# Kernel optimization log

Measured on AMD Instinct MI355X. Metric: run time of the kernel, lower is better.

## Reference

```python
import jax, jax.numpy as jnp
import numpy as np

N, C, S = 16, 512, 4096

def setup_inputs() -> dict:
    rng = jax.random.key(0)
    k1, k2, k3 = jax.random.split(rng, 3)
    return {
        "key": jax.random.normal(k1, (N, C, S), dtype=jnp.float32),
        "value": jax.random.normal(k2, (N, C, S), dtype=jnp.float32),
        "query": jax.random.normal(k3, (N, C, S), dtype=jnp.float32),
    }

def reference(key, value, query):
    KC = key.shape[1]
    # query.permute(0,2,1): [N, C, S] -> [N, S, C]
    # sim_map = bmm(key, query^T): [N, C, C], scaled by KC^-0.5
    sim = jnp.einsum("ncs,nds->ncd", key, query) * (KC ** -0.5)
    # softmax over dim=1 (first C axis)
    sim = jax.nn.softmax(sim, axis=1)
    # context = bmm(sim, value): [N, C, C] @ [N, C, S] -> [N, C, S]
    context = jnp.einsum("ncd,nds->ncs", sim, value)
    return context
```

## Files before the change

kernel.cpp:

```cpp
#include <hip/hip_runtime.h>

typedef __bf16 bf16x8 __attribute__((ext_vector_type(8)));
typedef float f32x4 __attribute__((ext_vector_type(4)));
typedef unsigned short u16;
typedef u16 u16x4 __attribute__((ext_vector_type(4)));
typedef u16 u16x8 __attribute__((ext_vector_type(8)));

__device__ __forceinline__ u16 f2bf(float f) {
  unsigned u = __builtin_bit_cast(unsigned, f);
  unsigned r = (u + 0x7fffu + ((u >> 16) & 1u)) >> 16;
  return (u16)r;
}

__device__ __forceinline__ void gld_lds16(const u16* g, u16* l) {
  __builtin_amdgcn_global_load_lds(
      (__attribute__((address_space(1))) void*)(g),
      (__attribute__((address_space(3))) void*)(l), 16, 0, 0);
}

__device__ __forceinline__ f32x4 ntload4(const float* p) {
  return __builtin_nontemporal_load((const f32x4*)p);
}

__global__ __launch_bounds__(256) void k_cvt(const float* __restrict__ K,
                                             const float* __restrict__ Q,
                                             u16* __restrict__ Kb,
                                             u16* __restrict__ Qb) {
  const float* src = blockIdx.y ? Q : K;
  u16* dst = blockIdx.y ? Qb : Kb;
  const size_t base = (size_t)blockIdx.x * 4096;
  const int t = threadIdx.x;
  f32x4 v[4];
#pragma unroll
  for (int c = 0; c < 4; ++c)
    v[c] = ntload4(src + base + c * 1024 + t * 4);
#pragma unroll
  for (int c = 0; c < 4; ++c) {
    u16x4 h;
    h[0] = f2bf(v[c][0]); h[1] = f2bf(v[c][1]); h[2] = f2bf(v[c][2]); h[3] = f2bf(v[c][3]);
    *(u16x4*)(dst + base + c * 1024 + t * 4) = h;
  }
}

__global__ __launch_bounds__(512) void k_mix(const u16* __restrict__ Kb,
                                             const u16* __restrict__ Qb,
                                             float* __restrict__ Lp,
                                             const float* __restrict__ V,
                                             u16* __restrict__ Vt) {
  extern __shared__ char raw[];
  const int bid = blockIdx.x;
  const int t = threadIdx.x;

  if (bid % 5 == 0) {
    u16* sA = (u16*)raw;
    u16* sB = (u16*)(raw + 32768);
    const int sid0 = bid / 5;
    const int sid = (sid0 & 7) * 64 + (sid0 >> 3);
    const int n = sid >> 5;
    const int rem = sid & 31;
    const int kc = rem >> 4;
    const int r2 = rem & 15;
    const int cy = r2 >> 2, dx = r2 & 3;
    const int lane = t & 63, wid = t >> 6;
    const int wr = wid >> 2, wc = wid & 3;
    const float scale = 0.04419417382415922f;

    const u16* Ab = Kb + ((size_t)n * 512 + cy * 128) * 4096 + kc * 2048;
    const u16* Bb = Qb + ((size_t)n * 512 + dx * 128) * 4096 + kc * 2048;
    f32x4 acc[4][2] = {};
    const int srow0 = t >> 3;
    const int scol = ((t & 7) << 3) ^ ((srow0 & 7) << 3);

#define MIX_STAGE(buf, k0)                                                      \
  {                                                                             \
    _Pragma("unroll") for (int q = 0; q < 2; ++q) {                             \
      const int row = q * 64 + srow0;                                           \
      gld_lds16(Ab + (size_t)row * 4096 + (k0) + scol,                          \
                sA + (buf) * 8192 + (q * 512 + (wid << 6)) * 8);                \
      gld_lds16(Bb + (size_t)row * 4096 + (k0) + scol,                          \
                sB + (buf) * 8192 + (q * 512 + (wid << 6)) * 8);                \
    }                                                                           \
  }
#define MIX_COMPUTE(buf)                                                        \
  {                                                                             \
    _Pragma("unroll") for (int ki = 0; ki < 2; ++ki) {                          \
      bf16x8 a[4], b[2];                                                        \
      const int ce = ki * 32 + (lane >> 4) * 8;                                 \
      _Pragma("unroll") for (int mi = 0; mi < 4; ++mi) {                        \
        const int r = wr * 64 + mi * 16 + (lane & 15);                          \
        a[mi] = *(const bf16x8*)&sA[(buf) * 8192 + r * 64 + (ce ^ ((r & 7) << 3))]; \
      }                                                                         \
      _Pragma("unroll") for (int ni = 0; ni < 2; ++ni) {                        \
        const int r = wc * 32 + ni * 16 + (lane & 15);                          \
        b[ni] = *(const bf16x8*)&sB[(buf) * 8192 + r * 64 + (ce ^ ((r & 7) << 3))]; \
      }                                                                         \
      __builtin_amdgcn_s_setprio(1);                                            \
      _Pragma("unroll") for (int mi = 0; mi < 4; ++mi)                          \
        _Pragma("unroll") for (int ni = 0; ni < 2; ++ni)                        \
          acc[mi][ni] = __builtin_amdgcn_mfma_f32_16x16x32_bf16(                \
              a[mi], b[ni], acc[mi][ni], 0, 0, 0);                              \
      __builtin_amdgcn_s_setprio(0);                                            \
    }                                                                           \
  }

    MIX_STAGE(0, 0);
    __syncthreads();
    int cur = 0;
    for (int kt = 0; kt < 31; ++kt) {
      MIX_STAGE(cur ^ 1, (kt + 1) << 6);
      MIX_COMPUTE(cur);
      __syncthreads();
      cur ^= 1;
    }
    MIX_COMPUTE(cur);

    float* Lb = Lp + ((size_t)kc * 16 + n) * 512 * 512;
    const int c0 = cy * 128, d0 = dx * 128;
#pragma unroll
    for (int mi = 0; mi < 4; ++mi)
#pragma unroll
      for (int ni = 0; ni < 2; ++ni) {
        int colo = d0 + wc * 32 + ni * 16 + (lane & 15);
#pragma unroll
        for (int j = 0; j < 4; ++j) {
          int rowo = c0 + wr * 64 + mi * 16 + ((lane >> 4) << 2) + j;
          Lb[(size_t)rowo * 512 + colo] = acc[mi][ni][j] * scale;
        }
      }
#undef MIX_STAGE
#undef MIX_COMPUTE
  } else {
    const int vid = bid - bid / 5 - 1;
    const int sub = t >> 8, tt = t & 255;
    const int tile = vid * 2 + sub;
    const int n = tile >> 8;
    const int r = tile & 255;
    const int d0 = (r >> 6) * 128, s0 = (r & 63) * 64;
    float* lds = (float*)(raw + sub * 34816);
    {
      const int r0 = tt >> 4, c4 = (tt & 15) << 2;
#pragma unroll
      for (int p = 0; p < 8; ++p) {
        const int dr = r0 + p * 16;
        f32x4 v = ntload4(V + ((size_t)n * 512 + d0 + dr) * 4096 + s0 + c4);
        const int sw = ((dr >> 3) & 7) << 2;
        *(f32x4*)(&lds[dr * 68 + (c4 ^ sw)]) = v;
      }
    }
    __syncthreads();
    {
      const int sr0 = tt >> 4, dcol = (tt & 15) << 3;
#pragma unroll
      for (int p2 = 0; p2 < 4; ++p2) {
        const int sr = sr0 + p2 * 16;
        u16x8 h;
#pragma unroll
        for (int j = 0; j < 8; ++j) {
          const int d = dcol + j;
          h[j] = f2bf(lds[d * 68 + (sr ^ (((d >> 3) & 7) << 2))]);
        }
        *(u16x8*)(Vt + ((size_t)n * 4096 + s0 + sr) * 512 + d0 + dcol) = h;
      }
    }
  }
}

template <int KDIV>
__global__ __launch_bounds__(256) void k_stats(const float* __restrict__ Lp,
                                               u16* __restrict__ E) {
  __shared__ float redm[8][32];
  __shared__ float reds[8][32];
  const int n = blockIdx.y;
  const int d0 = blockIdx.x * 32;
  const int tx = threadIdx.x & 31, ty = threadIdx.x >> 5;
  const size_t CH = (size_t)16 * 512 * 512;
  const float* B = Lp + (size_t)n * 512 * 512 + d0 + tx;

  float m = -3.0e38f, s = 0.f;
  for (int c = ty; c < 512; c += 8) {
    float v = B[(size_t)c * 512];
#pragma unroll
    for (int q = 1; q < KDIV; ++q) v += B[q * CH + (size_t)c * 512];
    float nm = fmaxf(m, v);
    s = s * __expf(m - nm) + __expf(v - nm);
    m = nm;
  }
  redm[ty][tx] = m;
  reds[ty][tx] = s;
  __syncthreads();
  float M = redm[0][tx];
#pragma unroll
  for (int q = 1; q < 8; ++q) M = fmaxf(M, redm[q][tx]);
  float S = 0.f;
#pragma unroll
  for (int q = 0; q < 8; ++q) S += reds[q][tx] * __expf(redm[q][tx] - M);
  const float si = 1.0f / S;

  u16* Eb = E + (size_t)n * 512 * 512 + d0 + tx;
  for (int c = ty; c < 512; c += 8) {
    float v = B[(size_t)c * 512];
#pragma unroll
    for (int q = 1; q < KDIV; ++q) v += B[q * CH + (size_t)c * 512];
    Eb[(size_t)c * 512] = f2bf(__expf(v - M) * si);
  }
}

template <int KDIV>
__global__ __launch_bounds__(512) void k_simk(const u16* __restrict__ Kb,
                                              const u16* __restrict__ Qb,
                                              float* __restrict__ Lp) {
  __shared__ u16 sA[2][128 * 64];
  __shared__ u16 sB[2][128 * 64];
  constexpr int NB = 256 * KDIV;
  const int bid = blockIdx.x;
  const int sid = (bid & 7) * (NB / 8) + (bid >> 3);
  constexpr int PER_N = 16 * KDIV;
  const int n = sid / PER_N;
  const int rem = sid % PER_N;
  const int kc = rem >> 4;
  const int r2 = rem & 15;
  const int cy = r2 >> 2, dx = r2 & 3;
  const int t = threadIdx.x, lane = t & 63, wid = t >> 6;
  const int wr = wid >> 2, wc = wid & 3;
  const float scale = 0.04419417382415922f;

  const u16* Ab = Kb + ((size_t)n * 512 + cy * 128) * 4096 + kc * (4096 / KDIV);
  const u16* Bb = Qb + ((size_t)n * 512 + dx * 128) * 4096 + kc * (4096 / KDIV);
  f32x4 acc[4][2] = {};
  const int srow0 = t >> 3;
  const int scol = ((t & 7) << 3) ^ ((srow0 & 7) << 3);

#define SIM_STAGE(buf, k0)                                                      \
  {                                                                             \
    _Pragma("unroll") for (int q = 0; q < 2; ++q) {                             \
      const int row = q * 64 + srow0;                                           \
      gld_lds16(Ab + (size_t)row * 4096 + (k0) + scol,                          \
                &sA[buf][(q * 512 + (wid << 6)) * 8]);                          \
      gld_lds16(Bb + (size_t)row * 4096 + (k0) + scol,                          \
                &sB[buf][(q * 512 + (wid << 6)) * 8]);                          \
    }                                                                           \
  }
#define SIM_COMPUTE(buf)                                                        \
  {                                                                             \
    _Pragma("unroll") for (int ki = 0; ki < 2; ++ki) {                          \
      bf16x8 a[4], b[2];                                                        \
      const int ce = ki * 32 + (lane >> 4) * 8;                                 \
      _Pragma("unroll") for (int mi = 0; mi < 4; ++mi) {                        \
        const int r = wr * 64 + mi * 16 + (lane & 15);                          \
        a[mi] = *(const bf16x8*)&sA[buf][r * 64 + (ce ^ ((r & 7) << 3))];       \
      }                                                                         \
      _Pragma("unroll") for (int ni = 0; ni < 2; ++ni) {                        \
        const int r = wc * 32 + ni * 16 + (lane & 15);                          \
        b[ni] = *(const bf16x8*)&sB[buf][r * 64 + (ce ^ ((r & 7) << 3))];       \
      }                                                                         \
      _Pragma("unroll") for (int mi = 0; mi < 4; ++mi)                          \
        _Pragma("unroll") for (int ni = 0; ni < 2; ++ni)                        \
          acc[mi][ni] = __builtin_amdgcn_mfma_f32_16x16x32_bf16(                \
              a[mi], b[ni], acc[mi][ni], 0, 0, 0);                              \
    }                                                                           \
  }

  constexpr int NSTEP = 64 / KDIV;
  SIM_STAGE(0, 0);
  __syncthreads();
  int cur = 0;
  for (int kt = 0; kt < NSTEP - 1; ++kt) {
    SIM_STAGE(cur ^ 1, (kt + 1) << 6);
    SIM_COMPUTE(cur);
    __syncthreads();
    cur ^= 1;
  }
  SIM_COMPUTE(cur);

  float* Lb = Lp + ((size_t)kc * 16 + n) * 512 * 512;
  const int c0 = cy * 128, d0 = dx * 128;
#pragma unroll
  for (int mi = 0; mi < 4; ++mi)
#pragma unroll
    for (int ni = 0; ni < 2; ++ni) {
      int colo = d0 + wc * 32 + ni * 16 + (lane & 15);
#pragma unroll
      for (int j = 0; j < 4; ++j) {
        int rowo = c0 + wr * 64 + mi * 16 + ((lane >> 4) << 2) + j;
        Lb[(size_t)rowo * 512 + colo] = acc[mi][ni][j] * scale;
      }
    }
#undef SIM_STAGE
#undef SIM_COMPUTE
}

__global__ __launch_bounds__(256) void k_vt(const float* __restrict__ V,
                                            u16* __restrict__ Vt) {
  __shared__ float lds[128 * 68];
  const int n = blockIdx.z, d0 = blockIdx.y * 128, s0 = blockIdx.x * 64;
  const int t = threadIdx.x;
  {
    const int r0 = t >> 4, c4 = (t & 15) << 2;
#pragma unroll
    for (int p = 0; p < 8; ++p) {
      const int dr = r0 + p * 16;
      f32x4 v = ntload4(V + ((size_t)n * 512 + d0 + dr) * 4096 + s0 + c4);
      const int sw = ((dr >> 3) & 7) << 2;
      *(f32x4*)(&lds[dr * 68 + (c4 ^ sw)]) = v;
    }
  }
  __syncthreads();
  {
    const int sr0 = t >> 4, dcol = (t & 15) << 3;
#pragma unroll
    for (int p2 = 0; p2 < 4; ++p2) {
      const int sr = sr0 + p2 * 16;
      u16x8 h;
#pragma unroll
      for (int j = 0; j < 8; ++j) {
        const int d = dcol + j;
        h[j] = f2bf(lds[d * 68 + (sr ^ (((d >> 3) & 7) << 2))]);
      }
      *(u16x8*)(Vt + ((size_t)n * 4096 + s0 + sr) * 512 + d0 + dcol) = h;
    }
  }
}

__global__ __launch_bounds__(512) void k_ctx3(const u16* __restrict__ E,
                                              const u16* __restrict__ Vt,
                                              float* __restrict__ O) {
  __shared__ u16 sA[2][128 * 64];
  __shared__ u16 sB[2][128 * 64];
  const int bid = blockIdx.x;
  const int sid = (bid & 7) * 256 + (bid >> 3);
  const int n = sid >> 7;
  const int rem = sid & 127;
  const int cy = rem >> 5, sx = rem & 31;
  const int t = threadIdx.x, lane = t & 63, wid = t >> 6;
  const int wr = wid >> 2, wc = wid & 3;

  const u16* Ab = E + ((size_t)n * 512 + cy * 128) * 512;
  const u16* Bb = Vt + ((size_t)n * 4096 + sx * 128) * 512;
  const int srow0 = t >> 3;
  const int scol = ((t & 7) << 3) ^ ((srow0 & 7) << 3);
  f32x4 acc[4][2] = {};

#define CTX_STAGE(buf, kd)                                                      \
  {                                                                             \
    _Pragma("unroll") for (int q = 0; q < 2; ++q) {                             \
      const int row = q * 64 + srow0;                                           \
      gld_lds16(Ab + (size_t)row * 512 + (kd) + scol,                           \
                &sA[buf][(q * 512 + (wid << 6)) * 8]);                          \
      gld_lds16(Bb + (size_t)row * 512 + (kd) + scol,                           \
                &sB[buf][(q * 512 + (wid << 6)) * 8]);                          \
    }                                                                           \
  }
#define CTX_COMPUTE(buf)                                                        \
  {                                                                             \
    _Pragma("unroll") for (int ki = 0; ki < 2; ++ki) {                          \
      bf16x8 a[4], b[2];                                                        \
      const int ce = ki * 32 + (lane >> 4) * 8;                                 \
      _Pragma("unroll") for (int mi = 0; mi < 4; ++mi) {                        \
        const int r = wr * 64 + mi * 16 + (lane & 15);                          \
        a[mi] = *(const bf16x8*)&sA[buf][r * 64 + (ce ^ ((r & 7) << 3))];       \
      }                                                                         \
      _Pragma("unroll") for (int ni = 0; ni < 2; ++ni) {                        \
        const int r = wc * 32 + ni * 16 + (lane & 15);                          \
        b[ni] = *(const bf16x8*)&sB[buf][r * 64 + (ce ^ ((r & 7) << 3))];       \
      }                                                                         \
      _Pragma("unroll") for (int mi = 0; mi < 4; ++mi)                          \
        _Pragma("unroll") for (int ni = 0; ni < 2; ++ni)                        \
          acc[mi][ni] = __builtin_amdgcn_mfma_f32_16x16x32_bf16(                \
              a[mi], b[ni], acc[mi][ni], 0, 0, 0);                              \
    }                                                                           \
  }

  CTX_STAGE(0, 0);
  __syncthreads();
  int cur = 0;
  for (int kt = 0; kt < 7; ++kt) {
    CTX_STAGE(cur ^ 1, (kt + 1) << 6);
    CTX_COMPUTE(cur);
    __syncthreads();
    cur ^= 1;
  }
  CTX_COMPUTE(cur);

  float* Ob = O + ((size_t)n * 512 + cy * 128) * 4096 + sx * 128;
#pragma unroll
  for (int mi = 0; mi < 4; ++mi)
#pragma unroll
    for (int ni = 0; ni < 2; ++ni) {
      int colo = wc * 32 + ni * 16 + (lane & 15);
#pragma unroll
      for (int j = 0; j < 4; ++j) {
        int rowo = wr * 64 + mi * 16 + ((lane >> 4) << 2) + j;
        __builtin_nontemporal_store(acc[mi][ni][j], &Ob[(size_t)rowo * 4096 + colo]);
      }
    }
#undef CTX_STAGE
#undef CTX_COMPUTE
}

extern "C" void kernel_launch(void* const* d_in, const int* in_sizes, int n_in,
                              void* d_out, int out_size, void* d_ws, size_t ws_size,
                              hipStream_t stream) {
  const float* Kp = (const float*)d_in[0];
  const float* Vp = (const float*)d_in[1];
  const float* Qp = (const float*)d_in[2];
  float* Op = (float*)d_out;
  char* ws = (char*)d_ws;
  const size_t MB = 1024 * 1024;

  if (ws_size >= 192 * MB) {
    u16* Kb = (u16*)ws;
    u16* Qb = (u16*)(ws + 64 * MB);
    u16* Vt = (u16*)(ws + 128 * MB);
    u16* E  = (u16*)(ws + 64 * MB);
    float* Lp = Op;

    k_cvt<<<dim3(8192, 2), 256, 0, stream>>>(Kp, Qp, Kb, Qb);
    k_mix<<<2560, 512, 69632, stream>>>(Kb, Qb, Lp, Vp, Vt);
    k_stats<2><<<dim3(16, 16), 256, 0, stream>>>(Lp, E);
    k_ctx3<<<2048, 512, 0, stream>>>(E, Vt, Op);
  } else if (ws_size >= 128 * MB) {
    u16* Kb = (u16*)ws;
    u16* Qb = (u16*)(ws + 64 * MB);
    u16* Vt = (u16*)ws;
    u16* E  = (u16*)(ws + 64 * MB);
    float* Lp = Op;

    k_cvt<<<dim3(8192, 2), 256, 0, stream>>>(Kp, Qp, Kb, Qb);
    k_simk<2><<<512, 512, 0, stream>>>(Kb, Qb, Lp);
    k_stats<2><<<dim3(16, 16), 256, 0, stream>>>(Lp, E);
    k_vt<<<dim3(64, 4, 16), 256, 0, stream>>>(Vp, Vt);
    k_ctx3<<<2048, 512, 0, stream>>>(E, Vt, Op);
  }
}
```

Measured before the change: 239.5 us.

## Fuse fp32-to-bf16 conversion of K/Q into the similarity GEMM and vectorize stats

Removes the separate K/Q conversion kernel and its bf16 workspace round trip. The mixed GEMM/transpose kernel now loads fp32 K and Q directly into registers, converts them to bf16 and writes them into a single-buffered LDS tile, with register prefetch of the next tile. The softmax stats kernel is also reworked so each thread handles four columns with vector loads and stores, using fewer blocks. In exchange the GEMM loses its async global-to-LDS double buffering and now reads twice the bytes per tile, and the stats kernel launches only 64 blocks.

```diff
diff --git a/kernel.cpp b/kernel.cpp
--- a/kernel.cpp
+++ b/kernel.cpp
@@ -12,6 +12,13 @@
   return (u16)r;
 }
 
+__device__ __forceinline__ bf16x8 cvt8v(f32x4 a, f32x4 b) {
+  bf16x8 h;
+  h[0] = (__bf16)a[0]; h[1] = (__bf16)a[1]; h[2] = (__bf16)a[2]; h[3] = (__bf16)a[3];
+  h[4] = (__bf16)b[0]; h[5] = (__bf16)b[1]; h[6] = (__bf16)b[2]; h[7] = (__bf16)b[3];
+  return h;
+}
+
 __device__ __forceinline__ void gld_lds16(const u16* g, u16* l) {
   __builtin_amdgcn_global_load_lds(
       (__attribute__((address_space(1))) void*)(g),
@@ -22,38 +29,18 @@
   return __builtin_nontemporal_load((const f32x4*)p);
 }
 
-__global__ __launch_bounds__(256) void k_cvt(const float* __restrict__ K,
-                                             const float* __restrict__ Q,
-                                             u16* __restrict__ Kb,
-                                             u16* __restrict__ Qb) {
-  const float* src = blockIdx.y ? Q : K;
-  u16* dst = blockIdx.y ? Qb : Kb;
-  const size_t base = (size_t)blockIdx.x * 4096;
-  const int t = threadIdx.x;
-  f32x4 v[4];
-#pragma unroll
-  for (int c = 0; c < 4; ++c)
-    v[c] = ntload4(src + base + c * 1024 + t * 4);
-#pragma unroll
-  for (int c = 0; c < 4; ++c) {
-    u16x4 h;
-    h[0] = f2bf(v[c][0]); h[1] = f2bf(v[c][1]); h[2] = f2bf(v[c][2]); h[3] = f2bf(v[c][3]);
-    *(u16x4*)(dst + base + c * 1024 + t * 4) = h;
-  }
-}
-
-__global__ __launch_bounds__(512) void k_mix(const u16* __restrict__ Kb,
-                                             const u16* __restrict__ Qb,
-                                             float* __restrict__ Lp,
-                                             const float* __restrict__ V,
-                                             u16* __restrict__ Vt) {
+__global__ __launch_bounds__(512) void k_mixf2(const float* __restrict__ K,
+                                               const float* __restrict__ Q,
+                                               float* __restrict__ Lp,
+                                               const float* __restrict__ V,
+                                               u16* __restrict__ Vt) {
   extern __shared__ char raw[];
   const int bid = blockIdx.x;
   const int t = threadIdx.x;
 
   if (bid % 5 == 0) {
     u16* sA = (u16*)raw;
-    u16* sB = (u16*)(raw + 32768);
+    u16* sB = (u16*)(raw + 16384);
     const int sid0 = bid / 5;
     const int sid = (sid0 & 7) * 64 + (sid0 >> 3);
     const int n = sid >> 5;
@@ -65,34 +52,50 @@
     const int wr = wid >> 2, wc = wid & 3;
     const float scale = 0.04419417382415922f;
 
-    const u16* Ab = Kb + ((size_t)n * 512 + cy * 128) * 4096 + kc * 2048;
-    const u16* Bb = Qb + ((size_t)n * 512 + dx * 128) * 4096 + kc * 2048;
+    const float* Ab = K + ((size_t)n * 512 + cy * 128) * 4096 + kc * 2048;
+    const float* Bb = Q + ((size_t)n * 512 + dx * 128) * 4096 + kc * 2048;
     f32x4 acc[4][2] = {};
-    const int srow0 = t >> 3;
-    const int scol = ((t & 7) << 3) ^ ((srow0 & 7) << 3);
-
-#define MIX_STAGE(buf, k0)                                                      \
-  {                                                                             \
-    _Pragma("unroll") for (int q = 0; q < 2; ++q) {                             \
-      const int row = q * 64 + srow0;                                           \
-      gld_lds16(Ab + (size_t)row * 4096 + (k0) + scol,                          \
-                sA + (buf) * 8192 + (q * 512 + (wid << 6)) * 8);                \
-      gld_lds16(Bb + (size_t)row * 4096 + (k0) + scol,                          \
-                sB + (buf) * 8192 + (q * 512 + (wid << 6)) * 8);                \
-    }                                                                           \
-  }
-#define MIX_COMPUTE(buf)                                                        \
+
+    const int r0 = t >> 3, col8 = (t & 7) << 3;
+    const int swz = col8 ^ ((r0 & 7) << 3);
+    u16* const wA0 = sA + r0 * 64 + swz;
+    u16* const wA1 = sA + (r0 + 64) * 64 + swz;
+    u16* const wB0 = sB + r0 * 64 + swz;
+    u16* const wB1 = sB + (r0 + 64) * 64 + swz;
+    f32x4 ra[4], rb[4];
+
+#define MF_LOAD(k0)                                                             \
+  {                                                                             \
+    const float* pa = Ab + (size_t)r0 * 4096 + (k0) + col8;                     \
+    ra[0] = *(const f32x4*)pa;                                                  \
+    ra[1] = *(const f32x4*)(pa + 4);                                            \
+    ra[2] = *(const f32x4*)(pa + 64 * 4096);                                    \
+    ra[3] = *(const f32x4*)(pa + 64 * 4096 + 4);                                \
+    const float* pb = Bb + (size_t)r0 * 4096 + (k0) + col8;                     \
+    rb[0] = *(const f32x4*)pb;                                                  \
+    rb[1] = *(const f32x4*)(pb + 4);                                            \
+    rb[2] = *(const f32x4*)(pb + 64 * 4096);                                    \
+    rb[3] = *(const f32x4*)(pb + 64 * 4096 + 4);                                \
+  }
+#define MF_WRITE()                                                              \
+  {                                                                             \
+    *(bf16x8*)wA0 = cvt8v(ra[0], ra[1]);                                        \
+    *(bf16x8*)wA1 = cvt8v(ra[2], ra[3]);                                        \
+    *(bf16x8*)wB0 = cvt8v(rb[0], rb[1]);                                        \
+    *(bf16x8*)wB1 = cvt8v(rb[2], rb[3]);                                        \
+  }
+#define MF_COMPUTE()                                                            \
   {                                                                             \
     _Pragma("unroll") for (int ki = 0; ki < 2; ++ki) {                          \
       bf16x8 a[4], b[2];                                                        \
       const int ce = ki * 32 + (lane >> 4) * 8;                                 \
       _Pragma("unroll") for (int mi = 0; mi < 4; ++mi) {                        \
         const int r = wr * 64 + mi * 16 + (lane & 15);                          \
-        a[mi] = *(const bf16x8*)&sA[(buf) * 8192 + r * 64 + (ce ^ ((r & 7) << 3))]; \
+        a[mi] = *(const bf16x8*)&sA[r * 64 + (ce ^ ((r & 7) << 3))];            \
       }                                                                         \
       _Pragma("unroll") for (int ni = 0; ni < 2; ++ni) {                        \
         const int r = wc * 32 + ni * 16 + (lane & 15);                          \
-        b[ni] = *(const bf16x8*)&sB[(buf) * 8192 + r * 64 + (ce ^ ((r & 7) << 3))]; \
+        b[ni] = *(const bf16x8*)&sB[r * 64 + (ce ^ ((r & 7) << 3))];            \
       }                                                                         \
       __builtin_amdgcn_s_setprio(1);                                            \
       _Pragma("unroll") for (int mi = 0; mi < 4; ++mi)                          \
@@ -103,16 +106,15 @@
     }                                                                           \
   }
 
-    MIX_STAGE(0, 0);
-    __syncthreads();
-    int cur = 0;
-    for (int kt = 0; kt < 31; ++kt) {
-      MIX_STAGE(cur ^ 1, (kt + 1) << 6);
-      MIX_COMPUTE(cur);
+    MF_LOAD(0);
+#pragma unroll 1
+    for (int kt = 0; kt < 32; ++kt) {
+      MF_WRITE();
       __syncthreads();
-      cur ^= 1;
-    }
-    MIX_COMPUTE(cur);
+      if (kt < 31) MF_LOAD((kt + 1) << 6);
+      MF_COMPUTE();
+      __syncthreads();
+    }
 
     float* Lb = Lp + ((size_t)kc * 16 + n) * 512 * 512;
     const int c0 = cy * 128, d0 = dx * 128;
@@ -127,8 +129,9 @@
           Lb[(size_t)rowo * 512 + colo] = acc[mi][ni][j] * scale;
         }
       }
-#undef MIX_STAGE
-#undef MIX_COMPUTE
+#undef MF_LOAD
+#undef MF_WRITE
+#undef MF_COMPUTE
   } else {
     const int vid = bid - bid / 5 - 1;
     const int sub = t >> 8, tt = t & 255;
@@ -166,42 +169,76 @@
 }
 
 template <int KDIV>
-__global__ __launch_bounds__(256) void k_stats(const float* __restrict__ Lp,
-                                               u16* __restrict__ E) {
-  __shared__ float redm[8][32];
-  __shared__ float reds[8][32];
+__global__ __launch_bounds__(256) void k_stats2(const float* __restrict__ Lp,
+                                                u16* __restrict__ E) {
+  __shared__ f32x4 redm[8][32];
+  __shared__ f32x4 reds[8][32];
   const int n = blockIdx.y;
-  const int d0 = blockIdx.x * 32;
   const int tx = threadIdx.x & 31, ty = threadIdx.x >> 5;
+  const int d0 = blockIdx.x * 128 + tx * 4;
   const size_t CH = (size_t)16 * 512 * 512;
-  const float* B = Lp + (size_t)n * 512 * 512 + d0 + tx;
-
-  float m = -3.0e38f, s = 0.f;
+  const float* B = Lp + (size_t)n * 512 * 512 + d0;
+
+  f32x4 m = {-3.0e38f, -3.0e38f, -3.0e38f, -3.0e38f};
+  f32x4 s = {0.f, 0.f, 0.f, 0.f};
   for (int c = ty; c < 512; c += 8) {
-    float v = B[(size_t)c * 512];
-#pragma unroll
-    for (int q = 1; q < KDIV; ++q) v += B[q * CH + (size_t)c * 512];
-    float nm = fmaxf(m, v);
-    s = s * __expf(m - nm) + __expf(v - nm);
-    m = nm;
+    f32x4 v = *(const f32x4*)(B + (size_t)c * 512);
+#pragma unroll
+    for (int q = 1; q < KDIV; ++q) v += *(const f32x4*)(B + q * CH + (size_t)c * 512);
+#pragma unroll
+    for (int j = 0; j < 4; ++j) {
+      float nm = fmaxf(m[j], v[j]);
+      s[j] = s[j] * __expf(m[j] - nm) + __expf(v[j] - nm);
+      m[j] = nm;
+    }
   }
   redm[ty][tx] = m;
   reds[ty][tx] = s;
   __syncthreads();
-  float M = redm[0][tx];
-#pragma unroll
-  for (int q = 1; q < 8; ++q) M = fmaxf(M, redm[q][tx]);
-  float S = 0.f;
-#pragma unroll
-  for (int q = 0; q < 8; ++q) S += reds[q][tx] * __expf(redm[q][tx] - M);
-  const float si = 1.0f / S;
-
-  u16* Eb = E + (size_t)n * 512 * 512 + d0 + tx;
+  f32x4 M = redm[0][tx], S;
+#pragma unroll
+  for (int q = 1; q < 8; ++q)
+#pragma unroll
+    for (int j = 0; j < 4; ++j) M[j] = fmaxf(M[j], redm[q][tx][j]);
+#pragma unroll
+  for (int j = 0; j < 4; ++j) S[j] = 0.f;
+#pragma unroll
+  for (int q = 0; q < 8; ++q)
+#pragma unroll
+    for (int j = 0; j < 4; ++j) S[j] += reds[q][tx][j] * __expf(redm[q][tx][j] - M[j]);
+  f32x4 si;
+#pragma unroll
+  for (int j = 0; j < 4; ++j) si[j] = 1.0f / S[j];
+
+  u16* Eb = E + (size_t)n * 512 * 512 + d0;
   for (int c = ty; c < 512; c += 8) {
-    float v = B[(size_t)c * 512];
-#pragma unroll
-    for (int q = 1; q < KDIV; ++q) v += B[q * CH + (size_t)c * 512];
-    Eb[(size_t)c * 512] = f2bf(__expf(v - M) * si);
+    f32x4 v = *(const f32x4*)(B + (size_t)c * 512);
+#pragma unroll
+    for (int q = 1; q < KDIV; ++q) v += *(const f32x4*)(B + q * CH + (size_t)c * 512);
+    u16x4 h;
+#pragma unroll
+    for (int j = 0; j < 4; ++j) h[j] = f2bf(__expf(v[j] - M[j]) * si[j]);
+    *(u16x4*)(Eb + (size_t)c * 512) = h;
+  }
+}
+
+__global__ __launch_bounds__(256) void k_cvt(const float* __restrict__ K,
+                                             const float* __restrict__ Q,
+                                             u16* __restrict__ Kb,
+                                             u16* __restrict__ Qb) {
+  const float* src = blockIdx.y ? Q : K;
+  u16* dst = blockIdx.y ? Qb : Kb;
+  const size_t base = (size_t)blockIdx.x * 4096;
+  const int t = threadIdx.x;
+  f32x4 v[4];
+#pragma unroll
+  for (int c = 0; c < 4; ++c)
+    v[c] = ntload4(src + base + c * 1024 + t * 4);
+#pragma unroll
+  for (int c = 0; c < 4; ++c) {
+    u16x4 h;
+    h[0] = f2bf(v[c][0]); h[1] = f2bf(v[c][1]); h[2] = f2bf(v[c][2]); h[3] = f2bf(v[c][3]);
+    *(u16x4*)(dst + base + c * 1024 + t * 4) = h;
   }
 }
 
@@ -407,28 +444,13 @@
   char* ws = (char*)d_ws;
   const size_t MB = 1024 * 1024;
 
-  if (ws_size >= 192 * MB) {
-    u16* Kb = (u16*)ws;
-    u16* Qb = (u16*)(ws + 64 * MB);
-    u16* Vt = (u16*)(ws + 128 * MB);
-    u16* E  = (u16*)(ws + 64 * MB);
-    float* Lp = Op;
-
-    k_cvt<<<dim3(8192, 2), 256, 0, stream>>>(Kp, Qp, Kb, Qb);
-    k_mix<<<2560, 512, 69632, stream>>>(Kb, Qb, Lp, Vp, Vt);
-    k_stats<2><<<dim3(16, 16), 256, 0, stream>>>(Lp, E);
-    k_ctx3<<<2048, 512, 0, stream>>>(E, Vt, Op);
-  } else if (ws_size >= 128 * MB) {
-    u16* Kb = (u16*)ws;
-    u16* Qb = (u16*)(ws + 64 * MB);
+  if (ws_size >= 72 * MB) {
     u16* Vt = (u16*)ws;
     u16* E  = (u16*)(ws + 64 * MB);
     float* Lp = Op;
 
-    k_cvt<<<dim3(8192, 2), 256, 0, stream>>>(Kp, Qp, Kb, Qb);
-    k_simk<2><<<512, 512, 0, stream>>>(Kb, Qb, Lp);
-    k_stats<2><<<dim3(16, 16), 256, 0, stream>>>(Lp, E);
-    k_vt<<<dim3(64, 4, 16), 256, 0, stream>>>(Vp, Vt);
+    k_mixf2<<<2560, 512, 69632, stream>>>(Kp, Qp, Lp, Vp, Vt);
+    k_stats2<2><<<dim3(4, 16), 256, 0, stream>>>(Lp, E);
     k_ctx3<<<2048, 512, 0, stream>>>(E, Vt, Op);
   }
 }
```

New measurement: 266.9 us. 11.4% more time.

## Make V-transpose blocks persistent in mixed kernel and vectorize softmax stats

Applied to the files above, without the earlier changes.

The mixed GEMM/transpose kernel now interleaves 512 GEMM blocks with 256 transpose blocks in a 2:1 pattern. Each transpose block loops over 16 tiles, so the launch drops from 2560 blocks to 768. This cuts block launch overhead and changes how the tensor-core GEMM work overlaps with the memory-bound V transpose. The stats kernel now processes four columns per thread with 128-bit loads and 64-bit bf16 stores, but launches only 64 blocks, so parallelism drops sharply.

```diff
diff --git a/kernel.cpp b/kernel.cpp
--- a/kernel.cpp
+++ b/kernel.cpp
@@ -42,19 +42,19 @@
   }
 }
 
-__global__ __launch_bounds__(512) void k_mix(const u16* __restrict__ Kb,
-                                             const u16* __restrict__ Qb,
-                                             float* __restrict__ Lp,
-                                             const float* __restrict__ V,
-                                             u16* __restrict__ Vt) {
+__global__ __launch_bounds__(512) void k_mix3(const u16* __restrict__ Kb,
+                                              const u16* __restrict__ Qb,
+                                              float* __restrict__ Lp,
+                                              const float* __restrict__ V,
+                                              u16* __restrict__ Vt) {
   extern __shared__ char raw[];
   const int bid = blockIdx.x;
   const int t = threadIdx.x;
 
-  if (bid % 5 == 0) {
+  if (bid % 3 != 2) {
     u16* sA = (u16*)raw;
     u16* sB = (u16*)(raw + 32768);
-    const int sid0 = bid / 5;
+    const int sid0 = (bid / 3) * 2 + (bid % 3);
     const int sid = (sid0 & 7) * 64 + (sid0 >> 3);
     const int n = sid >> 5;
     const int rem = sid & 31;
@@ -130,15 +130,17 @@
 #undef MIX_STAGE
 #undef MIX_COMPUTE
   } else {
-    const int vid = bid - bid / 5 - 1;
+    const int vid = bid / 3;
     const int sub = t >> 8, tt = t & 255;
-    const int tile = vid * 2 + sub;
-    const int n = tile >> 8;
-    const int r = tile & 255;
-    const int d0 = (r >> 6) * 128, s0 = (r & 63) * 64;
     float* lds = (float*)(raw + sub * 34816);
-    {
-      const int r0 = tt >> 4, c4 = (tt & 15) << 2;
+    const int r0 = tt >> 4, c4 = (tt & 15) << 2;
+    const int sr0 = tt >> 4, dcol = (tt & 15) << 3;
+#pragma unroll 1
+    for (int i = 0; i < 8; ++i) {
+      const int tile = vid * 16 + i * 2 + sub;
+      const int n = tile >> 8;
+      const int r = tile & 255;
+      const int d0 = (r >> 6) * 128, s0 = (r & 63) * 64;
 #pragma unroll
       for (int p = 0; p < 8; ++p) {
         const int dr = r0 + p * 16;
@@ -146,10 +148,7 @@
         const int sw = ((dr >> 3) & 7) << 2;
         *(f32x4*)(&lds[dr * 68 + (c4 ^ sw)]) = v;
       }
-    }
-    __syncthreads();
-    {
-      const int sr0 = tt >> 4, dcol = (tt & 15) << 3;
+      __syncthreads();
 #pragma unroll
       for (int p2 = 0; p2 < 4; ++p2) {
         const int sr = sr0 + p2 * 16;
@@ -161,47 +160,62 @@
         }
         *(u16x8*)(Vt + ((size_t)n * 4096 + s0 + sr) * 512 + d0 + dcol) = h;
       }
+      __syncthreads();
     }
   }
 }
 
 template <int KDIV>
-__global__ __launch_bounds__(256) void k_stats(const float* __restrict__ Lp,
-                                               u16* __restrict__ E) {
-  __shared__ float redm[8][32];
-  __shared__ float reds[8][32];
+__global__ __launch_bounds__(256) void k_stats2(const float* __restrict__ Lp,
+                                                u16* __restrict__ E) {
+  __shared__ f32x4 redm[8][32];
+  __shared__ f32x4 reds[8][32];
   const int n = blockIdx.y;
-  const int d0 = blockIdx.x * 32;
   const int tx = threadIdx.x & 31, ty = threadIdx.x >> 5;
+  const int d0 = blockIdx.x * 128 + tx * 4;
   const size_t CH = (size_t)16 * 512 * 512;
-  const float* B = Lp + (size_t)n * 512 * 512 + d0 + tx;
-
-  float m = -3.0e38f, s = 0.f;
+  const float* B = Lp + (size_t)n * 512 * 512 + d0;
+
+  f32x4 m = {-3.0e38f, -3.0e38f, -3.0e38f, -3.0e38f};
+  f32x4 s = {0.f, 0.f, 0.f, 0.f};
   for (int c = ty; c < 512; c += 8) {
-    float v = B[(size_t)c * 512];
-#pragma unroll
-    for (int q = 1; q < KDIV; ++q) v += B[q * CH + (size_t)c * 512];
-    float nm = fmaxf(m, v);
-    s = s * __expf(m - nm) + __expf(v - nm);
-    m = nm;
+    f32x4 v = *(const f32x4*)(B + (size_t)c * 512);
+#pragma unroll
+    for (int q = 1; q < KDIV; ++q) v += *(const f32x4*)(B + q * CH + (size_t)c * 512);
+#pragma unroll
+    for (int j = 0; j < 4; ++j) {
+      float nm = fmaxf(m[j], v[j]);
+      s[j] = s[j] * __expf(m[j] - nm) + __expf(v[j] - nm);
+      m[j] = nm;
+    }
   }
   redm[ty][tx] = m;
   reds[ty][tx] = s;
   __syncthreads();
-  float M = redm[0][tx];
-#pragma unroll
-  for (int q = 1; q < 8; ++q) M = fmaxf(M, redm[q][tx]);
-  float S = 0.f;
-#pragma unroll
-  for (int q = 0; q < 8; ++q) S += reds[q][tx] * __expf(redm[q][tx] - M);
-  const float si = 1.0f / S;
-
-  u16* Eb = E + (size_t)n * 512 * 512 + d0 + tx;
+  f32x4 M = redm[0][tx], S;
+#pragma unroll
+  for (int q = 1; q < 8; ++q)
+#pragma unroll
+    for (int j = 0; j < 4; ++j) M[j] = fmaxf(M[j], redm[q][tx][j]);
+#pragma unroll
+  for (int j = 0; j < 4; ++j) S[j] = 0.f;
+#pragma unroll
+  for (int q = 0; q < 8; ++q)
+#pragma unroll
+    for (int j = 0; j < 4; ++j) S[j] += reds[q][tx][j] * __expf(redm[q][tx][j] - M[j]);
+  f32x4 si;
+#pragma unroll
+  for (int j = 0; j < 4; ++j) si[j] = 1.0f / S[j];
+
+  u16* Eb = E + (size_t)n * 512 * 512 + d0;
   for (int c = ty; c < 512; c += 8) {
-    float v = B[(size_t)c * 512];
-#pragma unroll
-    for (int q = 1; q < KDIV; ++q) v += B[q * CH + (size_t)c * 512];
-    Eb[(size_t)c * 512] = f2bf(__expf(v - M) * si);
+    f32x4 v = *(const f32x4*)(B + (size_t)c * 512);
+#pragma unroll
+    for (int q = 1; q < KDIV; ++q) v += *(const f32x4*)(B + q * CH + (size_t)c * 512);
+    u16x4 h;
+#pragma unroll
+    for (int j = 0; j < 4; ++j) h[j] = f2bf(__expf(v[j] - M[j]) * si[j]);
+    *(u16x4*)(Eb + (size_t)c * 512) = h;
   }
 }
 
@@ -415,8 +429,8 @@
     float* Lp = Op;
 
     k_cvt<<<dim3(8192, 2), 256, 0, stream>>>(Kp, Qp, Kb, Qb);
-    k_mix<<<2560, 512, 69632, stream>>>(Kb, Qb, Lp, Vp, Vt);
-    k_stats<2><<<dim3(16, 16), 256, 0, stream>>>(Lp, E);
+    k_mix3<<<768, 512, 69632, stream>>>(Kb, Qb, Lp, Vp, Vt);
+    k_stats2<2><<<dim3(4, 16), 256, 0, stream>>>(Lp, E);
     k_ctx3<<<2048, 512, 0, stream>>>(E, Vt, Op);
   } else if (ws_size >= 128 * MB) {
     u16* Kb = (u16*)ws;
@@ -427,7 +441,7 @@
 
     k_cvt<<<dim3(8192, 2), 256, 0, stream>>>(Kp, Qp, Kb, Qb);
     k_simk<2><<<512, 512, 0, stream>>>(Kb, Qb, Lp);
-    k_stats<2><<<dim3(16, 16), 256, 0, stream>>>(Lp, E);
+    k_stats2<2><<<dim3(4, 16), 256, 0, stream>>>(Lp, E);
     k_vt<<<dim3(64, 4, 16), 256, 0, stream>>>(Vp, Vt);
     k_ctx3<<<2048, 512, 0, stream>>>(E, Vt, Op);
   }
```

Measured after the change: 254.5 us. +6.3%, slower.
